# Kernel optimization log

Hardware: AMD Instinct MI355X
Metric: run time of the kernel (lower is better)

## Reference

```python
import jax, jax.numpy as jnp
import numpy as np

B, N, D = 4, 2048, 768
OUT = 768

def setup_inputs() -> dict:
    key = jax.random.key(0)
    k1, k2 = jax.random.split(key)
    x = jax.random.normal(k1, (B, N, D), dtype=jnp.float32)
    kernel = jax.random.normal(k2, (3, D, OUT), dtype=jnp.float32) * 0.02
    return {"x": x, "kernel": kernel}

def reference(x, kernel):
    # Single-head attention with shared QKV kernel stack [3, D, OUT]
    q = jnp.einsum('bnd,do->bno', x, kernel[0])
    k = jnp.einsum('bnd,do->bno', x, kernel[1])
    v = jnp.einsum('bnd,do->bno', x, kernel[2])
    # NOTE: original divides by 64**0.5 == 8 regardless of dims (faithful)
    scores = jnp.einsum('bqo,bko->bqk', q, k) / 8.0
    attn = jax.nn.softmax(scores, axis=-1)
    return jnp.einsum('bqk,bko->bqo', attn, v)
```

## Files before the change

kernel.cpp:

```cpp
#include <hip/hip_runtime.h>
#include <hip/hip_bf16.h>

constexpr int B_ = 4, N_ = 2048, D_ = 768, OUT_ = 768;
constexpr int M_ = B_ * N_;

typedef __attribute__((ext_vector_type(8))) short short8;
typedef __attribute__((ext_vector_type(4))) float floatx4;

__device__ __forceinline__ unsigned short f2bfu(float f) {
    union { __hip_bfloat16 b; unsigned short u; } cv;
    cv.b = __float2bfloat16(f);
    return cv.u;
}

#define GLOAD_LDS16(g, l)                                                     \
    __builtin_amdgcn_global_load_lds(                                         \
        (const __attribute__((address_space(1))) void*)(g),                   \
        (__attribute__((address_space(3))) void*)(l), 16, 0, 0)

template <int BM>
__device__ __forceinline__ void gemm_core(
    const __hip_bfloat16* __restrict__ a_base, int lda,
    const __hip_bfloat16* __restrict__ b_base, int ldb,
    int m0, int n0, int K,
    __hip_bfloat16* As, __hip_bfloat16* Bs,
    floatx4 (&acc)[BM / 32][4]) {
    constexpr int MF = BM / 32;
    const int tid  = threadIdx.x;
    const int wave = tid >> 6, lane = tid & 63;
    const int wm = (wave >> 1) * (BM / 2), wn = (wave & 1) * 64;
    const int lrow = lane & 15, kq = lane >> 4;
    const int sw = lrow & 7;

    for (int k0 = 0; k0 < K; k0 += 64) {
#pragma unroll
        for (int i = 0; i < MF; ++i) {
            const int u = i * 256 + tid;
            const int row = u >> 3, cg = (u & 7) ^ (row & 7);
            const __hip_bfloat16* g =
                a_base + (size_t)(m0 + row) * lda + k0 + cg * 8;
            GLOAD_LDS16(g, As + (size_t)(i * 256 + wave * 64) * 8);
        }
#pragma unroll
        for (int i = 0; i < 4; ++i) {
            const int u = i * 256 + tid;
            const int row = u >> 3, cg = (u & 7) ^ (row & 7);
            const __hip_bfloat16* g =
                b_base + (size_t)(n0 + row) * ldb + k0 + cg * 8;
            GLOAD_LDS16(g, Bs + (size_t)(i * 256 + wave * 64) * 8);
        }
        __syncthreads();

#pragma unroll
        for (int s = 0; s < 2; ++s) {
            short8 af[MF], bfr[4];
#pragma unroll
            for (int t = 0; t < MF; ++t) {
                const int row = wm + t * 16 + lrow;
                const int slot = (s * 4 + kq) ^ sw;
                af[t] = *(const short8*)(As + row * 64 + slot * 8);
            }
#pragma unroll
            for (int t = 0; t < 4; ++t) {
                const int row = wn + t * 16 + lrow;
                const int slot = (s * 4 + kq) ^ sw;
                bfr[t] = *(const short8*)(Bs + row * 64 + slot * 8);
            }
#pragma unroll
            for (int mi = 0; mi < MF; ++mi)
#pragma unroll
                for (int ni = 0; ni < 4; ++ni)
                    acc[mi][ni] = __builtin_amdgcn_mfma_f32_16x16x32_bf16(
                        af[mi], bfr[ni], acc[mi][ni], 0, 0, 0);
        }
        __syncthreads();
    }
}

__global__ __launch_bounds__(256)
void convert_x(const float* __restrict__ x, __hip_bfloat16* __restrict__ xb) {
    const size_t i = (size_t)blockIdx.x * 2048 + (size_t)threadIdx.x * 8;
    float4 a = *(const float4*)(x + i);
    float4 b = *(const float4*)(x + i + 4);
    ushort4 pa = make_ushort4(f2bfu(a.x), f2bfu(a.y), f2bfu(a.z), f2bfu(a.w));
    ushort4 pb = make_ushort4(f2bfu(b.x), f2bfu(b.y), f2bfu(b.z), f2bfu(b.w));
    *(ushort4*)((unsigned short*)xb + i) = pa;
    *(ushort4*)((unsigned short*)xb + i + 4) = pb;
}

__global__ __launch_bounds__(256)
void transpose_w(const float* __restrict__ w, __hip_bfloat16* __restrict__ wt) {
    __shared__ float t[32][33];
    const int s = blockIdx.z;
    const int d0 = blockIdx.x * 32, o0 = blockIdx.y * 32;
    const int tx = threadIdx.x, ty = threadIdx.y;
    const float* ws = w + (size_t)s * D_ * OUT_;
    __hip_bfloat16* wts = wt + (size_t)s * OUT_ * D_;
#pragma unroll
    for (int i = 0; i < 4; ++i)
        t[ty + 8 * i][tx] = ws[(size_t)(d0 + ty + 8 * i) * OUT_ + o0 + tx];
    __syncthreads();
#pragma unroll
    for (int i = 0; i < 4; ++i)
        wts[(size_t)(o0 + ty + 8 * i) * D_ + d0 + tx] =
            __float2bfloat16(t[tx][ty + 8 * i]);
}

__global__ __launch_bounds__(256)
void qkv_mfma(const __hip_bfloat16* __restrict__ xb,
              const __hip_bfloat16* __restrict__ wt,
              __hip_bfloat16* __restrict__ q, __hip_bfloat16* __restrict__ k,
              __hip_bfloat16* __restrict__ vt) {
    __shared__ __align__(16) char smem[34816];
    __hip_bfloat16* As = (__hip_bfloat16*)smem;
    __hip_bfloat16* Bs = As + 128 * 64;
    const int s = blockIdx.z;
    const int m0 = blockIdx.x * 128, n0 = blockIdx.y * 128;
    floatx4 acc[4][4] = {};
    gemm_core<128>(xb, D_, wt + (size_t)s * OUT_ * D_, D_, m0, n0, D_, As, Bs,
                   acc);

    const int tid = threadIdx.x, wave = tid >> 6, lane = tid & 63;
    const int wm = (wave >> 1) * 64, wn = (wave & 1) * 64;
    const int lrow = lane & 15, kq = lane >> 4;
    unsigned short* E = (unsigned short*)smem;

    if (s < 2) {
#pragma unroll
        for (int mi = 0; mi < 4; ++mi)
#pragma unroll
            for (int ni = 0; ni < 4; ++ni) {
                const int n = wn + ni * 16 + lrow;
#pragma unroll
                for (int r = 0; r < 4; ++r)
                    E[(wm + mi * 16 + kq * 4 + r) * 136 + n] =
                        f2bfu(acc[mi][ni][r]);
            }
    } else {
#pragma unroll
        for (int mi = 0; mi < 4; ++mi)
#pragma unroll
            for (int ni = 0; ni < 4; ++ni) {
                const int n = wn + ni * 16 + lrow;
#pragma unroll
                for (int r = 0; r < 4; ++r)
                    E[n * 136 + wm + mi * 16 + kq * 4 + r] =
                        f2bfu(acc[mi][ni][r]);
            }
    }
    __syncthreads();

    if (s < 2) {
        __hip_bfloat16* out = (s == 0) ? q : k;
#pragma unroll
        for (int i = 0; i < 8; ++i) {
            const int u = i * 256 + tid, row = u >> 4, c = u & 15;
            short8 v = *(const short8*)(E + row * 136 + c * 8);
            *(short8*)(out + (size_t)(m0 + row) * OUT_ + n0 + c * 8) = v;
        }
    } else {
        const int b = m0 >> 11, j0 = m0 & 2047;
#pragma unroll
        for (int i = 0; i < 8; ++i) {
            const int u = i * 256 + tid, nrow = u >> 4, c = u & 15;
            short8 v = *(const short8*)(E + nrow * 136 + c * 8);
            *(short8*)(vt + ((size_t)b * OUT_ + n0 + nrow) * N_ + j0 + c * 8) =
                v;
        }
    }
}

__global__ __launch_bounds__(256)
void scores_mfma(const __hip_bfloat16* __restrict__ q,
                 const __hip_bfloat16* __restrict__ k,
                 float* __restrict__ S) {
    __shared__ __align__(16) __hip_bfloat16 As[128 * 64];
    __shared__ __align__(16) __hip_bfloat16 Bs[128 * 64];
    const int b = blockIdx.z;
    const int m0 = blockIdx.x * 128, n0 = blockIdx.y * 128;
    floatx4 acc[4][4] = {};
    gemm_core<128>(q + (size_t)b * N_ * OUT_, OUT_,
                   k + (size_t)b * N_ * OUT_, OUT_, m0, n0, OUT_, As, Bs, acc);

    const int tid = threadIdx.x, wave = tid >> 6, lane = tid & 63;
    const int wm = (wave >> 1) * 64, wn = (wave & 1) * 64;
    const int lrow = lane & 15, kq = lane >> 4;
    float* Sb = S + (size_t)b * N_ * N_;
#pragma unroll
    for (int mi = 0; mi < 4; ++mi)
#pragma unroll
        for (int ni = 0; ni < 4; ++ni) {
            const int j = n0 + wn + ni * 16 + lrow;
#pragma unroll
            for (int r = 0; r < 4; ++r) {
                const int i = m0 + wm + mi * 16 + kq * 4 + r;
                Sb[(size_t)i * N_ + j] = acc[mi][ni][r] * 0.125f;
            }
        }
}

__global__ __launch_bounds__(256)
void softmax_rows_bf16(float* __restrict__ S) {
    __shared__ float red[8];
    const int row = blockIdx.x;
    float* p = S + (size_t)row * (size_t)N_;
    const int tid = threadIdx.x;

    float4* p4 = (float4*)p;
    float4 a = p4[tid];
    float4 b = p4[tid + 256];

    float m = fmaxf(fmaxf(fmaxf(a.x, a.y), fmaxf(a.z, a.w)),
                    fmaxf(fmaxf(b.x, b.y), fmaxf(b.z, b.w)));
#pragma unroll
    for (int off = 32; off > 0; off >>= 1) m = fmaxf(m, __shfl_xor(m, off, 64));
    const int wid = tid >> 6, lane = tid & 63;
    if (lane == 0) red[wid] = m;
    __syncthreads();
    if (tid == 0) red[4] = fmaxf(fmaxf(red[0], red[1]), fmaxf(red[2], red[3]));
    __syncthreads();
    m = red[4];

    a.x = __expf(a.x - m); a.y = __expf(a.y - m);
    a.z = __expf(a.z - m); a.w = __expf(a.w - m);
    b.x = __expf(b.x - m); b.y = __expf(b.y - m);
    b.z = __expf(b.z - m); b.w = __expf(b.w - m);

    float s = a.x + a.y + a.z + a.w + b.x + b.y + b.z + b.w;
#pragma unroll
    for (int off = 32; off > 0; off >>= 1) s += __shfl_xor(s, off, 64);
    if (lane == 0) red[wid] = s;
    __syncthreads();
    if (tid == 0) red[5] = red[0] + red[1] + red[2] + red[3];
    __syncthreads();
    const float r = 1.0f / red[5];

    ushort4* o4 = (ushort4*)p;
    o4[tid] = make_ushort4(f2bfu(a.x * r), f2bfu(a.y * r),
                           f2bfu(a.z * r), f2bfu(a.w * r));
    o4[tid + 256] = make_ushort4(f2bfu(b.x * r), f2bfu(b.y * r),
                                 f2bfu(b.z * r), f2bfu(b.w * r));
}

__global__ __launch_bounds__(256)
void pv_mfma(const __hip_bfloat16* __restrict__ P,
             const __hip_bfloat16* __restrict__ vt,
             float* __restrict__ out) {
    __shared__ __align__(16) __hip_bfloat16 As[64 * 64];
    __shared__ __align__(16) __hip_bfloat16 Bs[128 * 64];
    const int b = blockIdx.z;
    const int m0 = blockIdx.x * 64, n0 = blockIdx.y * 128;
    floatx4 acc[2][4] = {};
    gemm_core<64>(P + (size_t)b * N_ * 4096, 4096,
                  vt + (size_t)b * OUT_ * N_, N_, m0, n0, N_, As, Bs, acc);

    const int tid = threadIdx.x, wave = tid >> 6, lane = tid & 63;
    const int wm = (wave >> 1) * 32, wn = (wave & 1) * 64;
    const int lrow = lane & 15, kq = lane >> 4;
#pragma unroll
    for (int mi = 0; mi < 2; ++mi)
#pragma unroll
        for (int ni = 0; ni < 4; ++ni) {
            const int n = n0 + wn + ni * 16 + lrow;
#pragma unroll
            for (int r = 0; r < 4; ++r) {
                const int i = m0 + wm + mi * 16 + kq * 4 + r;
                out[((size_t)b * N_ + i) * OUT_ + n] = acc[mi][ni][r];
            }
        }
}

extern "C" void kernel_launch(void* const* d_in, const int* in_sizes, int n_in,
                              void* d_out, int out_size, void* d_ws, size_t ws_size,
                              hipStream_t stream) {
    const float* x = (const float*)d_in[0];
    const float* w = (const float*)d_in[1];
    float* out = (float*)d_out;

    char* ws = (char*)d_ws;
    __hip_bfloat16* q  = (__hip_bfloat16*)ws;
    __hip_bfloat16* k  = q + (size_t)M_ * OUT_;
    __hip_bfloat16* vt = k + (size_t)M_ * OUT_;
    __hip_bfloat16* xb = vt + (size_t)M_ * OUT_;
    __hip_bfloat16* wt = xb + (size_t)M_ * D_;
    float* S = (float*)(ws + (size_t)3 * M_ * OUT_ * sizeof(__hip_bfloat16));

    convert_x<<<dim3(M_ * D_ / 2048), dim3(256), 0, stream>>>(x, xb);
    transpose_w<<<dim3(24, 24, 3), dim3(32, 8), 0, stream>>>(w, wt);
    qkv_mfma<<<dim3(M_ / 128, OUT_ / 128, 3), dim3(256), 0, stream>>>(xb, wt, q, k, vt);
    scores_mfma<<<dim3(N_ / 128, N_ / 128, B_), dim3(256), 0, stream>>>(q, k, S);
    softmax_rows_bf16<<<dim3(M_), dim3(256), 0, stream>>>(S);
    pv_mfma<<<dim3(N_ / 64, OUT_ / 128, B_), dim3(256), 0, stream>>>(
        (const __hip_bfloat16*)S, vt, out);
}
```

Measured before the change: 215.0 us.

## Double-buffer GEMM core with BK=32, shrink tiles to 64x128, fuse prep kernels

New measurement: 243.1 us. +13.1%, slower.

```diff
diff --git a/kernel.cpp b/kernel.cpp
--- a/kernel.cpp
+++ b/kernel.cpp
@@ -19,91 +19,98 @@
         (__attribute__((address_space(3))) void*)(l), 16, 0, 0)
 
 template <int BM>
-__device__ __forceinline__ void gemm_core(
+__device__ __forceinline__ void gemm_core_db(
     const __hip_bfloat16* __restrict__ a_base, int lda,
     const __hip_bfloat16* __restrict__ b_base, int ldb,
     int m0, int n0, int K,
     __hip_bfloat16* As, __hip_bfloat16* Bs,
     floatx4 (&acc)[BM / 32][4]) {
-    constexpr int MF = BM / 32;
     const int tid  = threadIdx.x;
     const int wave = tid >> 6, lane = tid & 63;
     const int wm = (wave >> 1) * (BM / 2), wn = (wave & 1) * 64;
     const int lrow = lane & 15, kq = lane >> 4;
-    const int sw = lrow & 7;
-
-    for (int k0 = 0; k0 < K; k0 += 64) {
-#pragma unroll
-        for (int i = 0; i < MF; ++i) {
+
+    auto stage = [&](int buf, int k0) {
+#pragma unroll
+        for (int i = 0; i < BM / 64; ++i) {
             const int u = i * 256 + tid;
-            const int row = u >> 3, cg = (u & 7) ^ (row & 7);
+            const int row = u >> 2;
+            const int cg = (u & 3) ^ ((row + (row >> 2)) & 3);
             const __hip_bfloat16* g =
                 a_base + (size_t)(m0 + row) * lda + k0 + cg * 8;
-            GLOAD_LDS16(g, As + (size_t)(i * 256 + wave * 64) * 8);
-        }
-#pragma unroll
-        for (int i = 0; i < 4; ++i) {
+            GLOAD_LDS16(g, As + buf * (BM * 32) + (i * 256 + wave * 64) * 8);
+        }
+#pragma unroll
+        for (int i = 0; i < 2; ++i) {
             const int u = i * 256 + tid;
-            const int row = u >> 3, cg = (u & 7) ^ (row & 7);
+            const int row = u >> 2;
+            const int cg = (u & 3) ^ ((row + (row >> 2)) & 3);
             const __hip_bfloat16* g =
                 b_base + (size_t)(n0 + row) * ldb + k0 + cg * 8;
-            GLOAD_LDS16(g, Bs + (size_t)(i * 256 + wave * 64) * 8);
-        }
-        __syncthreads();
-
-#pragma unroll
-        for (int s = 0; s < 2; ++s) {
-            short8 af[MF], bfr[4];
-#pragma unroll
-            for (int t = 0; t < MF; ++t) {
-                const int row = wm + t * 16 + lrow;
-                const int slot = (s * 4 + kq) ^ sw;
-                af[t] = *(const short8*)(As + row * 64 + slot * 8);
-            }
-#pragma unroll
-            for (int t = 0; t < 4; ++t) {
-                const int row = wn + t * 16 + lrow;
-                const int slot = (s * 4 + kq) ^ sw;
-                bfr[t] = *(const short8*)(Bs + row * 64 + slot * 8);
-            }
-#pragma unroll
-            for (int mi = 0; mi < MF; ++mi)
-#pragma unroll
-                for (int ni = 0; ni < 4; ++ni)
-                    acc[mi][ni] = __builtin_amdgcn_mfma_f32_16x16x32_bf16(
-                        af[mi], bfr[ni], acc[mi][ni], 0, 0, 0);
-        }
-        __syncthreads();
+            GLOAD_LDS16(g, Bs + buf * (128 * 32) + (i * 256 + wave * 64) * 8);
+        }
+    };
+
+    stage(0, 0);
+    int buf = 0;
+    for (int k0 = 0; k0 < K; k0 += 32) {
+        __syncthreads();
+        if (k0 + 32 < K) stage(buf ^ 1, k0 + 32);
+
+        const __hip_bfloat16* Ab = As + buf * (BM * 32);
+        const __hip_bfloat16* Bb = Bs + buf * (128 * 32);
+        short8 af[BM / 32], bfr[4];
+#pragma unroll
+        for (int t = 0; t < BM / 32; ++t) {
+            const int row = wm + t * 16 + lrow;
+            const int slot = kq ^ ((row + (row >> 2)) & 3);
+            af[t] = *(const short8*)(Ab + row * 32 + slot * 8);
+        }
+#pragma unroll
+        for (int t = 0; t < 4; ++t) {
+            const int row = wn + t * 16 + lrow;
+            const int slot = kq ^ ((row + (row >> 2)) & 3);
+            bfr[t] = *(const short8*)(Bb + row * 32 + slot * 8);
+        }
+#pragma unroll
+        for (int mi = 0; mi < BM / 32; ++mi)
+#pragma unroll
+            for (int ni = 0; ni < 4; ++ni)
+                acc[mi][ni] = __builtin_amdgcn_mfma_f32_16x16x32_bf16(
+                    af[mi], bfr[ni], acc[mi][ni], 0, 0, 0);
+        buf ^= 1;
     }
 }
 
 __global__ __launch_bounds__(256)
-void convert_x(const float* __restrict__ x, __hip_bfloat16* __restrict__ xb) {
-    const size_t i = (size_t)blockIdx.x * 2048 + (size_t)threadIdx.x * 8;
-    float4 a = *(const float4*)(x + i);
-    float4 b = *(const float4*)(x + i + 4);
-    ushort4 pa = make_ushort4(f2bfu(a.x), f2bfu(a.y), f2bfu(a.z), f2bfu(a.w));
-    ushort4 pb = make_ushort4(f2bfu(b.x), f2bfu(b.y), f2bfu(b.z), f2bfu(b.w));
-    *(ushort4*)((unsigned short*)xb + i) = pa;
-    *(ushort4*)((unsigned short*)xb + i + 4) = pb;
-}
-
-__global__ __launch_bounds__(256)
-void transpose_w(const float* __restrict__ w, __hip_bfloat16* __restrict__ wt) {
+void prep(const float* __restrict__ x, const float* __restrict__ w,
+          __hip_bfloat16* __restrict__ xb, __hip_bfloat16* __restrict__ wt) {
     __shared__ float t[32][33];
-    const int s = blockIdx.z;
-    const int d0 = blockIdx.x * 32, o0 = blockIdx.y * 32;
-    const int tx = threadIdx.x, ty = threadIdx.y;
-    const float* ws = w + (size_t)s * D_ * OUT_;
-    __hip_bfloat16* wts = wt + (size_t)s * OUT_ * D_;
-#pragma unroll
-    for (int i = 0; i < 4; ++i)
-        t[ty + 8 * i][tx] = ws[(size_t)(d0 + ty + 8 * i) * OUT_ + o0 + tx];
-    __syncthreads();
-#pragma unroll
-    for (int i = 0; i < 4; ++i)
-        wts[(size_t)(o0 + ty + 8 * i) * D_ + d0 + tx] =
-            __float2bfloat16(t[tx][ty + 8 * i]);
+    const int tid = threadIdx.x;
+    if (blockIdx.x < 3072) {
+        const size_t i = (size_t)blockIdx.x * 2048 + (size_t)tid * 8;
+        float4 a = *(const float4*)(x + i);
+        float4 b = *(const float4*)(x + i + 4);
+        *(ushort4*)((unsigned short*)xb + i) =
+            make_ushort4(f2bfu(a.x), f2bfu(a.y), f2bfu(a.z), f2bfu(a.w));
+        *(ushort4*)((unsigned short*)xb + i + 4) =
+            make_ushort4(f2bfu(b.x), f2bfu(b.y), f2bfu(b.z), f2bfu(b.w));
+    } else {
+        const int bid = blockIdx.x - 3072;
+        const int s = bid / 576, rem = bid % 576;
+        const int d0 = (rem / 24) * 32, o0 = (rem % 24) * 32;
+        const int tx = tid & 31, ty = tid >> 5;
+        const float* ws = w + (size_t)s * D_ * OUT_;
+        __hip_bfloat16* wts = wt + (size_t)s * OUT_ * D_;
+#pragma unroll
+        for (int i = 0; i < 4; ++i)
+            t[ty + 8 * i][tx] = ws[(size_t)(d0 + ty + 8 * i) * OUT_ + o0 + tx];
+        __syncthreads();
+#pragma unroll
+        for (int i = 0; i < 4; ++i)
+            wts[(size_t)(o0 + ty + 8 * i) * D_ + d0 + tx] =
+                __float2bfloat16(t[tx][ty + 8 * i]);
+    }
 }
 
 __global__ __launch_bounds__(256)
@@ -111,23 +118,24 @@
               const __hip_bfloat16* __restrict__ wt,
               __hip_bfloat16* __restrict__ q, __hip_bfloat16* __restrict__ k,
               __hip_bfloat16* __restrict__ vt) {
-    __shared__ __align__(16) char smem[34816];
+    __shared__ __align__(16) char smem[24576];
     __hip_bfloat16* As = (__hip_bfloat16*)smem;
-    __hip_bfloat16* Bs = As + 128 * 64;
+    __hip_bfloat16* Bs = (__hip_bfloat16*)(smem + 8192);
     const int s = blockIdx.z;
-    const int m0 = blockIdx.x * 128, n0 = blockIdx.y * 128;
-    floatx4 acc[4][4] = {};
-    gemm_core<128>(xb, D_, wt + (size_t)s * OUT_ * D_, D_, m0, n0, D_, As, Bs,
-                   acc);
+    const int m0 = blockIdx.x * 64, n0 = blockIdx.y * 128;
+    floatx4 acc[2][4] = {};
+    gemm_core_db<64>(xb, D_, wt + (size_t)s * OUT_ * D_, D_, m0, n0, D_, As,
+                     Bs, acc);
 
     const int tid = threadIdx.x, wave = tid >> 6, lane = tid & 63;
-    const int wm = (wave >> 1) * 64, wn = (wave & 1) * 64;
+    const int wm = (wave >> 1) * 32, wn = (wave & 1) * 64;
     const int lrow = lane & 15, kq = lane >> 4;
     unsigned short* E = (unsigned short*)smem;
+    __syncthreads();
 
     if (s < 2) {
 #pragma unroll
-        for (int mi = 0; mi < 4; ++mi)
+        for (int mi = 0; mi < 2; ++mi)
 #pragma unroll
             for (int ni = 0; ni < 4; ++ni) {
                 const int n = wn + ni * 16 + lrow;
@@ -136,34 +144,30 @@
                     E[(wm + mi * 16 + kq * 4 + r) * 136 + n] =
                         f2bfu(acc[mi][ni][r]);
             }
-    } else {
-#pragma unroll
-        for (int mi = 0; mi < 4; ++mi)
-#pragma unroll
-            for (int ni = 0; ni < 4; ++ni) {
-                const int n = wn + ni * 16 + lrow;
-#pragma unroll
-                for (int r = 0; r < 4; ++r)
-                    E[n * 136 + wm + mi * 16 + kq * 4 + r] =
-                        f2bfu(acc[mi][ni][r]);
-            }
-    }
-    __syncthreads();
-
-    if (s < 2) {
+        __syncthreads();
         __hip_bfloat16* out = (s == 0) ? q : k;
 #pragma unroll
-        for (int i = 0; i < 8; ++i) {
+        for (int i = 0; i < 4; ++i) {
             const int u = i * 256 + tid, row = u >> 4, c = u & 15;
             short8 v = *(const short8*)(E + row * 136 + c * 8);
             *(short8*)(out + (size_t)(m0 + row) * OUT_ + n0 + c * 8) = v;
         }
     } else {
+#pragma unroll
+        for (int mi = 0; mi < 2; ++mi)
+#pragma unroll
+            for (int ni = 0; ni < 4; ++ni) {
+                const int n = wn + ni * 16 + lrow;
+                *(ushort4*)(E + n * 88 + wm + mi * 16 + kq * 4) =
+                    make_ushort4(f2bfu(acc[mi][ni][0]), f2bfu(acc[mi][ni][1]),
+                                 f2bfu(acc[mi][ni][2]), f2bfu(acc[mi][ni][3]));
+            }
+        __syncthreads();
         const int b = m0 >> 11, j0 = m0 & 2047;
 #pragma unroll
-        for (int i = 0; i < 8; ++i) {
-            const int u = i * 256 + tid, nrow = u >> 4, c = u & 15;
-            short8 v = *(const short8*)(E + nrow * 136 + c * 8);
+        for (int i = 0; i < 4; ++i) {
+            const int u = i * 256 + tid, nrow = u >> 3, c = u & 7;
+            short8 v = *(const short8*)(E + nrow * 88 + c * 8);
             *(short8*)(vt + ((size_t)b * OUT_ + n0 + nrow) * N_ + j0 + c * 8) =
                 v;
         }
@@ -174,20 +178,21 @@
 void scores_mfma(const __hip_bfloat16* __restrict__ q,
                  const __hip_bfloat16* __restrict__ k,
                  float* __restrict__ S) {
-    __shared__ __align__(16) __hip_bfloat16 As[128 * 64];
-    __shared__ __align__(16) __hip_bfloat16 Bs[128 * 64];
+    __shared__ __align__(16) __hip_bfloat16 As[2 * 64 * 32];
+    __shared__ __align__(16) __hip_bfloat16 Bs[2 * 128 * 32];
     const int b = blockIdx.z;
-    const int m0 = blockIdx.x * 128, n0 = blockIdx.y * 128;
-    floatx4 acc[4][4] = {};
-    gemm_core<128>(q + (size_t)b * N_ * OUT_, OUT_,
-                   k + (size_t)b * N_ * OUT_, OUT_, m0, n0, OUT_, As, Bs, acc);
+    const int m0 = blockIdx.x * 64, n0 = blockIdx.y * 128;
+    floatx4 acc[2][4] = {};
+    gemm_core_db<64>(q + (size_t)b * N_ * OUT_, OUT_,
+                     k + (size_t)b * N_ * OUT_, OUT_, m0, n0, OUT_, As, Bs,
+                     acc);
 
     const int tid = threadIdx.x, wave = tid >> 6, lane = tid & 63;
-    const int wm = (wave >> 1) * 64, wn = (wave & 1) * 64;
+    const int wm = (wave >> 1) * 32, wn = (wave & 1) * 64;
     const int lrow = lane & 15, kq = lane >> 4;
     float* Sb = S + (size_t)b * N_ * N_;
 #pragma unroll
-    for (int mi = 0; mi < 4; ++mi)
+    for (int mi = 0; mi < 2; ++mi)
 #pragma unroll
         for (int ni = 0; ni < 4; ++ni) {
             const int j = n0 + wn + ni * 16 + lrow;
@@ -246,13 +251,13 @@
 void pv_mfma(const __hip_bfloat16* __restrict__ P,
              const __hip_bfloat16* __restrict__ vt,
              float* __restrict__ out) {
-    __shared__ __align__(16) __hip_bfloat16 As[64 * 64];
-    __shared__ __align__(16) __hip_bfloat16 Bs[128 * 64];
+    __shared__ __align__(16) __hip_bfloat16 As[2 * 64 * 32];
+    __shared__ __align__(16) __hip_bfloat16 Bs[2 * 128 * 32];
     const int b = blockIdx.z;
     const int m0 = blockIdx.x * 64, n0 = blockIdx.y * 128;
     floatx4 acc[2][4] = {};
-    gemm_core<64>(P + (size_t)b * N_ * 4096, 4096,
-                  vt + (size_t)b * OUT_ * N_, N_, m0, n0, N_, As, Bs, acc);
+    gemm_core_db<64>(P + (size_t)b * N_ * 4096, 4096,
+                     vt + (size_t)b * OUT_ * N_, N_, m0, n0, N_, As, Bs, acc);
 
     const int tid = threadIdx.x, wave = tid >> 6, lane = tid & 63;
     const int wm = (wave >> 1) * 32, wn = (wave & 1) * 64;
@@ -285,10 +290,9 @@
     __hip_bfloat16* wt = xb + (size_t)M_ * D_;
     float* S = (float*)(ws + (size_t)3 * M_ * OUT_ * sizeof(__hip_bfloat16));
 
-    convert_x<<<dim3(M_ * D_ / 2048), dim3(256), 0, stream>>>(x, xb);
-    transpose_w<<<dim3(24, 24, 3), dim3(32, 8), 0, stream>>>(w, wt);
-    qkv_mfma<<<dim3(M_ / 128, OUT_ / 128, 3), dim3(256), 0, stream>>>(xb, wt, q, k, vt);
-    scores_mfma<<<dim3(N_ / 128, N_ / 128, B_), dim3(256), 0, stream>>>(q, k, S);
+    prep<<<dim3(4800), dim3(256), 0, stream>>>(x, w, xb, wt);
+    qkv_mfma<<<dim3(M_ / 64, OUT_ / 128, 3), dim3(256), 0, stream>>>(xb, wt, q, k, vt);
+    scores_mfma<<<dim3(N_ / 64, N_ / 128, B_), dim3(256), 0, stream>>>(q, k, S);
     softmax_rows_bf16<<<dim3(M_), dim3(256), 0, stream>>>(S);
     pv_mfma<<<dim3(N_ / 64, OUT_ / 128, B_), dim3(256), 0, stream>>>(
         (const __hip_bfloat16*)S, vt, out);
```
